# Optimization experiments

Hardware: AMD Instinct MI355X
Metric: run time of the kernel (lower is better)

The kernel has to match this reference:

```python
import jax, jax.numpy as jnp
import numpy as np

INPUT_SIZE = 1024
HIDDEN_SIZE = 1024
BATCH = 4096


def setup_inputs() -> dict:
    key = jax.random.key(0)
    ks = jax.random.split(key, 20)
    k = 1.0 / HIDDEN_SIZE
    bound = float(np.sqrt(k))

    def u(kk, shape):
        return jax.random.uniform(kk, shape, jnp.float32, -bound, bound)

    inp = {
        "x": jax.random.normal(ks[0], (BATCH, INPUT_SIZE), jnp.float32),
        "h0": jax.random.normal(ks[1], (BATCH, HIDDEN_SIZE), jnp.float32),
        "c0": jax.random.normal(ks[2], (BATCH, HIDDEN_SIZE), jnp.float32),
        "W_ii": u(ks[3], (INPUT_SIZE, HIDDEN_SIZE)), "b_ii": u(ks[4], (HIDDEN_SIZE,)),
        "W_if": u(ks[5], (INPUT_SIZE, HIDDEN_SIZE)), "b_if": u(ks[6], (HIDDEN_SIZE,)),
        "W_ig": u(ks[7], (INPUT_SIZE, HIDDEN_SIZE)), "b_ig": u(ks[8], (HIDDEN_SIZE,)),
        "W_io": u(ks[9], (INPUT_SIZE, HIDDEN_SIZE)), "b_io": u(ks[10], (HIDDEN_SIZE,)),
        "W_hi": u(ks[11], (HIDDEN_SIZE, HIDDEN_SIZE)), "b_hi": u(ks[12], (HIDDEN_SIZE,)),
        "W_hf": u(ks[13], (HIDDEN_SIZE, HIDDEN_SIZE)), "b_hf": u(ks[14], (HIDDEN_SIZE,)),
        "W_hg": u(ks[15], (HIDDEN_SIZE, HIDDEN_SIZE)), "b_hg": u(ks[16], (HIDDEN_SIZE,)),
        "W_ho": u(ks[17], (HIDDEN_SIZE, HIDDEN_SIZE)), "b_ho": u(ks[18], (HIDDEN_SIZE,)),
    }
    return inp


def reference(x, h0, c0,
              W_ii, b_ii, W_if, b_if, W_ig, b_ig, W_io, b_io,
              W_hi, b_hi, W_hf, b_hf, W_hg, b_hg, W_ho, b_ho):
    # Fuse the 4 input-side and 4 hidden-side GEMMs into two wide GEMMs,
    # then a single fused gate computation — same math as the original.
    Wi = jnp.concatenate([W_ii, W_if, W_ig, W_io], axis=1)  # [In, 4H]
    Wh = jnp.concatenate([W_hi, W_hf, W_hg, W_ho], axis=1)  # [H, 4H]
    b = jnp.concatenate([b_ii + b_hi, b_if + b_hf, b_ig + b_hg, b_io + b_ho])
    gates = x @ Wi + h0 @ Wh + b  # [B, 4H]
    zi, zf, zg, zo = jnp.split(gates, 4, axis=1)
    i = jax.nn.sigmoid(zi)
    f = jax.nn.sigmoid(zf)
    g = jnp.tanh(zg)
    o = jax.nn.sigmoid(zo)
    c1 = f * c0 + i * g
    h1 = o * c1
    return h1, c1
```

## Files before the change

kernel.cpp:

```cpp
#include <hip/hip_runtime.h>

typedef unsigned short u16;
typedef unsigned int u32;
typedef __attribute__((ext_vector_type(8))) short short8;
typedef __attribute__((ext_vector_type(4))) float f32x4;

__device__ __forceinline__ u16 f2b(float f) {
  u32 u = __builtin_bit_cast(u32, f);
  u32 r = (u + 0x7FFFu + ((u >> 16) & 1u)) >> 16;
  return (u16)r;
}

__device__ __forceinline__ void gl_lds16(const void* g, void* l) {
  __builtin_amdgcn_global_load_lds(
      (const __attribute__((address_space(1))) u32*)g,
      (__attribute__((address_space(3))) u32*)l, 16, 0, 0);
}

struct Ptrs8 { const float* p[8]; };

__global__ __launch_bounds__(256) void wt_pack(Ptrs8 w, u16* __restrict__ Wt) {
  __shared__ float lds[64 * 64];
  const int tid = threadIdx.x;
  const int bid = blockIdx.x;
  const int mat = bid >> 8;
  const int g = mat & 3, h = mat >> 2;
  const int tile = bid & 255;
  const int kt = tile >> 4, nt = tile & 15;
  const float* __restrict__ src = w.p[mat];

#pragma unroll
  for (int i = 0; i < 4; ++i) {
    int c = tid + i * 256;
    int k = c >> 4, n4 = (c & 15) * 4;
    gl_lds16(src + (size_t)(kt * 64 + k) * 1024 + nt * 64 + n4, &lds[c * 4]);
  }
  asm volatile("s_waitcnt vmcnt(0)");
  __syncthreads();

#pragma unroll
  for (int i = 0; i < 2; ++i) {
    int c = tid + i * 256;
    int n = c & 63, kb = (c >> 6) * 8;
    short8 v;
#pragma unroll
    for (int j = 0; j < 8; ++j) v[j] = (short)f2b(lds[(kb + j) * 64 + n]);
    size_t off = (size_t)(g * 1024 + nt * 64 + n) * 2048 + h * 1024 + kt * 64 + kb;
    *reinterpret_cast<short8*>(Wt + off) = v;
  }
}

__global__ __launch_bounds__(256) void xh_pack(const float* __restrict__ x,
                                               const float* __restrict__ h0,
                                               u16* __restrict__ Ap) {
  int t = blockIdx.x * 256 + threadIdx.x;
  int m = t >> 8, kc = t & 255;
  const float* src = (kc < 128) ? (x + (size_t)m * 1024 + kc * 8)
                                : (h0 + (size_t)m * 1024 + (kc - 128) * 8);
  float4 a = *reinterpret_cast<const float4*>(src);
  float4 b = *reinterpret_cast<const float4*>(src + 4);
  short8 v;
  v[0] = (short)f2b(a.x); v[1] = (short)f2b(a.y);
  v[2] = (short)f2b(a.z); v[3] = (short)f2b(a.w);
  v[4] = (short)f2b(b.x); v[5] = (short)f2b(b.y);
  v[6] = (short)f2b(b.z); v[7] = (short)f2b(b.w);
  *reinterpret_cast<short8*>(Ap + (size_t)m * 2048 + kc * 8) = v;
}

__global__ void bias_pack(Ptrs8 b, float* __restrict__ bias) {
  int i = blockIdx.x * 1024 + threadIdx.x;
  int g = i >> 10, n = i & 1023;
  bias[i] = b.p[g][n] + b.p[4 + g][n];
}

#define LD8(base, off) (*reinterpret_cast<const short8*>((base) + (off)))
#define MFMA_(a, b, c) __builtin_amdgcn_mfma_f32_16x16x32_bf16(a, b, c, 0, 0, 0)

#define READ_A(DST, BASE)                                   \
  _Pragma("unroll")                                         \
  for (int mi = 0; mi < 4; ++mi) {                          \
    DST[mi][0] = LD8(Ab, arow + (BASE + mi) * 1024 + c0k);  \
    DST[mi][1] = LD8(Ab, arow + (BASE + mi) * 1024 + c1k);  \
  }
#define READ_B(DST, GB)                                     \
  _Pragma("unroll")                                         \
  for (int g = 0; g < 2; ++g) {                             \
    DST[g][0] = LD8(Bb, bbase + (GB + g) * 4096 + c0k);     \
    DST[g][1] = LD8(Bb, bbase + (GB + g) * 4096 + c1k);     \
  }
#define MFMA_QUAD(AF, BF, MO, GO)                                              \
  _Pragma("unroll")                                                            \
  for (int mi = 0; mi < 4; ++mi)                                               \
    _Pragma("unroll")                                                          \
    for (int g = 0; g < 2; ++g) {                                              \
      acc[MO + mi][GO + g] = MFMA_(AF[mi][0], BF[g][0], acc[MO + mi][GO + g]); \
      acc[MO + mi][GO + g] = MFMA_(AF[mi][1], BF[g][1], acc[MO + mi][GO + g]); \
    }

__global__ __launch_bounds__(512, 2) void lstm_fused(
    const u16* __restrict__ Ap, const float* __restrict__ c0,
    const u16* __restrict__ Wt, const float* __restrict__ bias,
    float* __restrict__ out) {
  __shared__ u16 As[2][256 * 64];
  __shared__ u16 Bs[2][256 * 64];

  const int tid = threadIdx.x;
  const int lane = tid & 63;
  const int wid = tid >> 6;
  const int wr = wid >> 2;
  const int wc = wid & 3;
  const int fl = lane & 15;
  const int hi = lane >> 4;
  const int lo7 = fl & 7;

  const int bid0 = blockIdx.x;
  const int sbid = (bid0 & 7) * 32 + (bid0 >> 3);
  const int m0 = (sbid >> 4) * 256;
  const int n0 = (sbid & 15) * 64;

  int aoff[4], boff[4];
#pragma unroll
  for (int i = 0; i < 4; ++i) {
    const int L = tid + i * 512;
    const int r = L >> 3, cL = L & 7;
    const int cg = cL ^ (r & 7);
    aoff[i] = (m0 + r) * 2048 + cg * 8;
    const int ge = r >> 6, wce = (r >> 4) & 3, ue = r & 15;
    boff[i] = (ge * 1024 + n0 + wce * 16 + ue) * 2048 + cg * 8;
  }

  auto stage = [&](int buf, int t) {
    const int k0 = t * 64;
#pragma unroll
    for (int i = 0; i < 4; ++i)
      gl_lds16(Ap + aoff[i] + k0, &As[buf][(tid + i * 512) * 8]);
#pragma unroll
    for (int i = 0; i < 4; ++i)
      gl_lds16(Wt + boff[i] + k0, &Bs[buf][(tid + i * 512) * 8]);
  };

  const int c0k = (hi ^ lo7) * 8;
  const int c1k = ((4 + hi) ^ lo7) * 8;
  const int arow = (wr * 128 + fl) * 64;
  const int bbase = (wc * 16 + fl) * 64;

  f32x4 acc[8][4] = {};

  stage(0, 0);

  for (int t = 0; t < 32; ++t) {
    const int cur = t & 1, nxt = cur ^ 1;
    const u16* Ab = &As[cur][0];
    const u16* Bb = &Bs[cur][0];

    asm volatile("s_waitcnt vmcnt(0)" ::: "memory");
    __builtin_amdgcn_s_barrier();

    short8 af03[4][2], af47[4][2], bf01[2][2], bf23[2][2];
    READ_B(bf01, 0)
    READ_A(af03, 0)
    READ_A(af47, 4)
    READ_B(bf23, 2)

    if (t < 31) stage(nxt, t + 1);

    MFMA_QUAD(af03, bf01, 0, 0)
    MFMA_QUAD(af47, bf01, 4, 0)
    MFMA_QUAD(af03, bf23, 0, 2)
    MFMA_QUAD(af47, bf23, 4, 2)
  }

  const int col = n0 + wc * 16 + fl;
  float bv[4];
#pragma unroll
  for (int g = 0; g < 4; ++g) bv[g] = bias[g * 1024 + col];

#pragma unroll
  for (int mi = 0; mi < 8; ++mi) {
#pragma unroll
    for (int r = 0; r < 4; ++r) {
      const int row = m0 + wr * 128 + mi * 16 + hi * 4 + r;
      const float zi = acc[mi][0][r] + bv[0];
      const float zf = acc[mi][1][r] + bv[1];
      const float zg = acc[mi][2][r] + bv[2];
      const float zo = acc[mi][3][r] + bv[3];
      const float ig = 1.f / (1.f + __expf(-zi));
      const float fg = 1.f / (1.f + __expf(-zf));
      const float gg = 1.f - 2.f / (__expf(2.f * zg) + 1.f);
      const float og = 1.f / (1.f + __expf(-zo));
      const float c0v = c0[(size_t)row * 1024 + col];
      const float c1 = fg * c0v + ig * gg;
      const float h1 = og * c1;
      out[(size_t)row * 1024 + col] = h1;
      out[(size_t)4194304 + (size_t)row * 1024 + col] = c1;
    }
  }
}

extern "C" void kernel_launch(void* const* d_in, const int* in_sizes, int n_in,
                              void* d_out, int out_size, void* d_ws, size_t ws_size,
                              hipStream_t stream) {
  const float* x  = (const float*)d_in[0];
  const float* h0 = (const float*)d_in[1];
  const float* c0 = (const float*)d_in[2];
  Ptrs8 w, b;
  for (int i = 0; i < 4; ++i) {
    w.p[i]     = (const float*)d_in[3 + 2 * i];
    b.p[i]     = (const float*)d_in[4 + 2 * i];
    w.p[4 + i] = (const float*)d_in[11 + 2 * i];
    b.p[4 + i] = (const float*)d_in[12 + 2 * i];
  }
  u16* Wt = (u16*)d_ws;
  u16* Ap = (u16*)((char*)d_ws + (size_t)4096 * 2048 * 2);
  float* bias = (float*)((char*)d_ws + (size_t)2 * 4096 * 2048 * 2);
  float* out = (float*)d_out;

  wt_pack<<<2048, 256, 0, stream>>>(w, Wt);
  xh_pack<<<4096, 256, 0, stream>>>(x, h0, Ap);
  bias_pack<<<4, 1024, 0, stream>>>(b, bias);
  lstm_fused<<<256, 512, 0, stream>>>(Ap, c0, Wt, bias, out);
}
```

Measured before the change: 94.39 us.

## Restructure GEMM main loop into phased ping-pong with split staging and priority

Replaces the simple double-buffered K loop, which waited on all loads, with a two-tile-ahead prefetch in the same buffer. Each K-tile is split into four MFMA phases separated by barriers. Global-to-LDS loads are split into halves and interleaved between the phases, partial vmcnt waits keep loads in flight, and s_setprio raises wave priority during MFMA bursts. The aim is to overlap memory latency with matrix math and keep waves in lockstep, at the cost of many extra barriers.

```diff
diff --git a/kernel.cpp b/kernel.cpp
--- a/kernel.cpp
+++ b/kernel.cpp
@@ -75,6 +75,11 @@
 
 #define LD8(base, off) (*reinterpret_cast<const short8*>((base) + (off)))
 #define MFMA_(a, b, c) __builtin_amdgcn_mfma_f32_16x16x32_bf16(a, b, c, 0, 0, 0)
+#define PIN asm volatile("" ::: "memory")
+#define SB0 __builtin_amdgcn_sched_barrier(0)
+#define BARR __builtin_amdgcn_s_barrier()
+#define PRIO1 __builtin_amdgcn_s_setprio(1);
+#define PRIO0 __builtin_amdgcn_s_setprio(0);
 
 #define READ_A(DST, BASE)                                   \
   _Pragma("unroll")                                         \
@@ -97,6 +102,42 @@
       acc[MO + mi][GO + g] = MFMA_(AF[mi][1], BF[g][1], acc[MO + mi][GO + g]); \
     }
 
+#define TILE4(BUF, T, ST, TAILW)                                             \
+  {                                                                          \
+    const u16* Ab = &As[BUF][0];                                             \
+    const u16* Bb = &Bs[BUF][0];                                             \
+    short8 af03[4][2], af47[4][2], bf01[2][2], bf23[2][2];                   \
+                                               \
+    READ_A(af03, 0) READ_B(bf01, 0) PIN;                                     \
+    BARR;                                                                    \
+    asm volatile("s_waitcnt lgkmcnt(0)"); SB0;                               \
+    PRIO1 MFMA_QUAD(af03, bf01, 0, 0) PRIO0                                  \
+    BARR; PIN;                                                               \
+                                 \
+    READ_B(bf23, 2) PIN;                                                     \
+    if (ST) { stageA(BUF, (T) + 2, 0); stageB(BUF, (T) + 2, 0); }            \
+    PIN;                                                                     \
+    BARR;                                                                    \
+    asm volatile("s_waitcnt lgkmcnt(0)"); SB0;                               \
+    PRIO1 MFMA_QUAD(af03, bf23, 0, 2) PRIO0                                  \
+    BARR; PIN;                                                               \
+                                     \
+    READ_A(af47, 4) PIN;                                                     \
+    if (ST) { stageB(BUF, (T) + 2, 1); }                                     \
+    PIN;                                                                     \
+    BARR;                                                                    \
+    asm volatile("s_waitcnt lgkmcnt(0)"); SB0;                               \
+    PRIO1 MFMA_QUAD(af47, bf01, 4, 0) PRIO0                                  \
+    BARR; PIN;                                                               \
+                                       \
+    if (ST) { stageA(BUF, (T) + 2, 1); }                                     \
+    PIN;                                                                     \
+    PRIO1 MFMA_QUAD(af47, bf23, 4, 2) PRIO0                                  \
+    if ((TAILW) == 8) asm volatile("s_waitcnt vmcnt(8)" ::: "memory");       \
+    else if ((TAILW) == 0) asm volatile("s_waitcnt vmcnt(0)" ::: "memory");  \
+    BARR; PIN;                                                               \
+  }
+
 __global__ __launch_bounds__(512, 2) void lstm_fused(
     const u16* __restrict__ Ap, const float* __restrict__ c0,
     const u16* __restrict__ Wt, const float* __restrict__ bias,
@@ -129,14 +170,15 @@
     boff[i] = (ge * 1024 + n0 + wce * 16 + ue) * 2048 + cg * 8;
   }
 
-  auto stage = [&](int buf, int t) {
+  auto stageA = [&](int buf, int t, int h) {
     const int k0 = t * 64;
-#pragma unroll
-    for (int i = 0; i < 4; ++i)
-      gl_lds16(Ap + aoff[i] + k0, &As[buf][(tid + i * 512) * 8]);
-#pragma unroll
-    for (int i = 0; i < 4; ++i)
-      gl_lds16(Wt + boff[i] + k0, &Bs[buf][(tid + i * 512) * 8]);
+    gl_lds16(Ap + aoff[h] + k0, &As[buf][(tid + h * 512) * 8]);
+    gl_lds16(Ap + aoff[h + 2] + k0, &As[buf][(tid + (h + 2) * 512) * 8]);
+  };
+  auto stageB = [&](int buf, int t, int h) {
+    const int k0 = t * 64;
+    gl_lds16(Wt + boff[2 * h] + k0, &Bs[buf][(tid + (2 * h) * 512) * 8]);
+    gl_lds16(Wt + boff[2 * h + 1] + k0, &Bs[buf][(tid + (2 * h + 1) * 512) * 8]);
   };
 
   const int c0k = (hi ^ lo7) * 8;
@@ -146,29 +188,17 @@
 
   f32x4 acc[8][4] = {};
 
-  stage(0, 0);
-
-  for (int t = 0; t < 32; ++t) {
-    const int cur = t & 1, nxt = cur ^ 1;
-    const u16* Ab = &As[cur][0];
-    const u16* Bb = &Bs[cur][0];
-
-    asm volatile("s_waitcnt vmcnt(0)" ::: "memory");
-    __builtin_amdgcn_s_barrier();
-
-    short8 af03[4][2], af47[4][2], bf01[2][2], bf23[2][2];
-    READ_B(bf01, 0)
-    READ_A(af03, 0)
-    READ_A(af47, 4)
-    READ_B(bf23, 2)
-
-    if (t < 31) stage(nxt, t + 1);
-
-    MFMA_QUAD(af03, bf01, 0, 0)
-    MFMA_QUAD(af47, bf01, 4, 0)
-    MFMA_QUAD(af03, bf23, 0, 2)
-    MFMA_QUAD(af47, bf23, 4, 2)
-  }
+  stageA(0, 0, 0); stageB(0, 0, 0); stageB(0, 0, 1); stageA(0, 0, 1);
+  stageA(1, 1, 0); stageB(1, 1, 0); stageB(1, 1, 1); stageA(1, 1, 1);
+  asm volatile("s_waitcnt vmcnt(8)" ::: "memory");
+  BARR; PIN;
+
+  for (int i = 0; i < 15; ++i) {
+    TILE4(0, 2 * i, 1, 8)
+    TILE4(1, 2 * i + 1, 1, 8)
+  }
+  TILE4(0, 30, 0, 0)
+  TILE4(1, 31, 0, -1)
 
   const int col = n0 + wc * 16 + fl;
   float bv[4];
```

Result: no change. 92.72 us (-1.8%).

## Merge pack kernels and retile LSTM GEMM with triple-buffered K=32 pipeline

Applied to the files above, without the earlier changes.

Folds the three prepack kernels into one launch so there is less launch overhead. Retiles the fused GEMM to 256-thread blocks of 256x32 outputs (512 blocks) with K-steps of 32, and replaces double buffering with a three-stage LDS ring that keeps two loads in flight under a partial vmcnt wait. The aim is more blocks for occupancy and better latency hiding. In exchange there are twice as many barriers, each K-step does less MFMA work, and the narrower N tile lowers B reuse per block.

```diff
diff --git a/kernel.cpp b/kernel.cpp
--- a/kernel.cpp
+++ b/kernel.cpp
@@ -19,155 +19,149 @@
 
 struct Ptrs8 { const float* p[8]; };
 
-__global__ __launch_bounds__(256) void wt_pack(Ptrs8 w, u16* __restrict__ Wt) {
+__global__ __launch_bounds__(256) void prepack(Ptrs8 w, Ptrs8 b,
+                                               const float* __restrict__ x,
+                                               const float* __restrict__ h0,
+                                               u16* __restrict__ Wt,
+                                               u16* __restrict__ Ap,
+                                               float* __restrict__ bias) {
   __shared__ float lds[64 * 64];
   const int tid = threadIdx.x;
   const int bid = blockIdx.x;
-  const int mat = bid >> 8;
-  const int g = mat & 3, h = mat >> 2;
-  const int tile = bid & 255;
-  const int kt = tile >> 4, nt = tile & 15;
-  const float* __restrict__ src = w.p[mat];
-
-#pragma unroll
-  for (int i = 0; i < 4; ++i) {
-    int c = tid + i * 256;
-    int k = c >> 4, n4 = (c & 15) * 4;
-    gl_lds16(src + (size_t)(kt * 64 + k) * 1024 + nt * 64 + n4, &lds[c * 4]);
-  }
-  asm volatile("s_waitcnt vmcnt(0)");
-  __syncthreads();
-
-#pragma unroll
-  for (int i = 0; i < 2; ++i) {
-    int c = tid + i * 256;
-    int n = c & 63, kb = (c >> 6) * 8;
+
+  if (bid < 2048) {
+    const int mat = bid >> 8;
+    const int g = mat & 3, h = mat >> 2;
+    const int tile = bid & 255;
+    const int kt = tile >> 4, nt = tile & 15;
+    const float* __restrict__ src = w.p[mat];
+#pragma unroll
+    for (int i = 0; i < 4; ++i) {
+      int c = tid + i * 256;
+      int k = c >> 4, n4 = (c & 15) * 4;
+      gl_lds16(src + (size_t)(kt * 64 + k) * 1024 + nt * 64 + n4, &lds[c * 4]);
+    }
+    asm volatile("s_waitcnt vmcnt(0)");
+    __syncthreads();
+#pragma unroll
+    for (int i = 0; i < 2; ++i) {
+      int c = tid + i * 256;
+      int n = c & 63, kb = (c >> 6) * 8;
+      short8 v;
+#pragma unroll
+      for (int j = 0; j < 8; ++j) v[j] = (short)f2b(lds[(kb + j) * 64 + n]);
+      size_t off = (size_t)(g * 1024 + nt * 64 + n) * 2048 + h * 1024 + kt * 64 + kb;
+      *reinterpret_cast<short8*>(Wt + off) = v;
+    }
+  } else if (bid < 6144) {
+    int t = (bid - 2048) * 256 + tid;
+    int m = t >> 8, kc = t & 255;
+    const float* src = (kc < 128) ? (x + (size_t)m * 1024 + kc * 8)
+                                  : (h0 + (size_t)m * 1024 + (kc - 128) * 8);
+    float4 a = *reinterpret_cast<const float4*>(src);
+    float4 bb = *reinterpret_cast<const float4*>(src + 4);
     short8 v;
-#pragma unroll
-    for (int j = 0; j < 8; ++j) v[j] = (short)f2b(lds[(kb + j) * 64 + n]);
-    size_t off = (size_t)(g * 1024 + nt * 64 + n) * 2048 + h * 1024 + kt * 64 + kb;
-    *reinterpret_cast<short8*>(Wt + off) = v;
-  }
-}
-
-__global__ __launch_bounds__(256) void xh_pack(const float* __restrict__ x,
-                                               const float* __restrict__ h0,
-                                               u16* __restrict__ Ap) {
-  int t = blockIdx.x * 256 + threadIdx.x;
-  int m = t >> 8, kc = t & 255;
-  const float* src = (kc < 128) ? (x + (size_t)m * 1024 + kc * 8)
-                                : (h0 + (size_t)m * 1024 + (kc - 128) * 8);
-  float4 a = *reinterpret_cast<const float4*>(src);
-  float4 b = *reinterpret_cast<const float4*>(src + 4);
-  short8 v;
-  v[0] = (short)f2b(a.x); v[1] = (short)f2b(a.y);
-  v[2] = (short)f2b(a.z); v[3] = (short)f2b(a.w);
-  v[4] = (short)f2b(b.x); v[5] = (short)f2b(b.y);
-  v[6] = (short)f2b(b.z); v[7] = (short)f2b(b.w);
-  *reinterpret_cast<short8*>(Ap + (size_t)m * 2048 + kc * 8) = v;
-}
-
-__global__ void bias_pack(Ptrs8 b, float* __restrict__ bias) {
-  int i = blockIdx.x * 1024 + threadIdx.x;
-  int g = i >> 10, n = i & 1023;
-  bias[i] = b.p[g][n] + b.p[4 + g][n];
+    v[0] = (short)f2b(a.x); v[1] = (short)f2b(a.y);
+    v[2] = (short)f2b(a.z); v[3] = (short)f2b(a.w);
+    v[4] = (short)f2b(bb.x); v[5] = (short)f2b(bb.y);
+    v[6] = (short)f2b(bb.z); v[7] = (short)f2b(bb.w);
+    *reinterpret_cast<short8*>(Ap + (size_t)m * 2048 + kc * 8) = v;
+  } else {
+    int i = (bid - 6144) * 256 + tid;
+    int g = i >> 10, n = i & 1023;
+    bias[i] = b.p[g][n] + b.p[4 + g][n];
+  }
 }
 
 #define LD8(base, off) (*reinterpret_cast<const short8*>((base) + (off)))
 #define MFMA_(a, b, c) __builtin_amdgcn_mfma_f32_16x16x32_bf16(a, b, c, 0, 0, 0)
 
-#define READ_A(DST, BASE)                                   \
-  _Pragma("unroll")                                         \
-  for (int mi = 0; mi < 4; ++mi) {                          \
-    DST[mi][0] = LD8(Ab, arow + (BASE + mi) * 1024 + c0k);  \
-    DST[mi][1] = LD8(Ab, arow + (BASE + mi) * 1024 + c1k);  \
-  }
-#define READ_B(DST, GB)                                     \
-  _Pragma("unroll")                                         \
-  for (int g = 0; g < 2; ++g) {                             \
-    DST[g][0] = LD8(Bb, bbase + (GB + g) * 4096 + c0k);     \
-    DST[g][1] = LD8(Bb, bbase + (GB + g) * 4096 + c1k);     \
-  }
-#define MFMA_QUAD(AF, BF, MO, GO)                                              \
-  _Pragma("unroll")                                                            \
-  for (int mi = 0; mi < 4; ++mi)                                               \
-    _Pragma("unroll")                                                          \
-    for (int g = 0; g < 2; ++g) {                                              \
-      acc[MO + mi][GO + g] = MFMA_(AF[mi][0], BF[g][0], acc[MO + mi][GO + g]); \
-      acc[MO + mi][GO + g] = MFMA_(AF[mi][1], BF[g][1], acc[MO + mi][GO + g]); \
-    }
-
-__global__ __launch_bounds__(512, 2) void lstm_fused(
+__global__ __launch_bounds__(256, 2) void lstm_fused(
     const u16* __restrict__ Ap, const float* __restrict__ c0,
     const u16* __restrict__ Wt, const float* __restrict__ bias,
     float* __restrict__ out) {
-  __shared__ u16 As[2][256 * 64];
-  __shared__ u16 Bs[2][256 * 64];
+  __shared__ u16 As[3][256 * 32];
+  __shared__ u16 Bs[3][128 * 32];
 
   const int tid = threadIdx.x;
   const int lane = tid & 63;
   const int wid = tid >> 6;
-  const int wr = wid >> 2;
-  const int wc = wid & 3;
+  const int wr = wid >> 1;
+  const int wc = wid & 1;
   const int fl = lane & 15;
   const int hi = lane >> 4;
-  const int lo7 = fl & 7;
 
   const int bid0 = blockIdx.x;
-  const int sbid = (bid0 & 7) * 32 + (bid0 >> 3);
-  const int m0 = (sbid >> 4) * 256;
-  const int n0 = (sbid & 15) * 64;
-
-  int aoff[4], boff[4];
+  const int sbid = (bid0 & 7) * 64 + (bid0 >> 3);
+  const int m0 = (sbid >> 5) * 256;
+  const int n0 = (sbid & 31) * 32;
+
+  int aoff[4], boff[2];
 #pragma unroll
   for (int i = 0; i < 4; ++i) {
-    const int L = tid + i * 512;
-    const int r = L >> 3, cL = L & 7;
-    const int cg = cL ^ (r & 7);
-    aoff[i] = (m0 + r) * 2048 + cg * 8;
-    const int ge = r >> 6, wce = (r >> 4) & 3, ue = r & 15;
+    const int c = tid + i * 256;
+    const int row = c >> 2, cL = c & 3;
+    const int cg = cL ^ ((row >> 2) & 3);
+    aoff[i] = (m0 + row) * 2048 + cg * 8;
+  }
+#pragma unroll
+  for (int i = 0; i < 2; ++i) {
+    const int c = tid + i * 256;
+    const int row = c >> 2, cL = c & 3;
+    const int cg = cL ^ ((row >> 2) & 3);
+    const int ge = row >> 5, rem = row & 31;
+    const int wce = rem >> 4, ue = rem & 15;
     boff[i] = (ge * 1024 + n0 + wce * 16 + ue) * 2048 + cg * 8;
   }
 
   auto stage = [&](int buf, int t) {
-    const int k0 = t * 64;
+    const int k0 = t * 32;
 #pragma unroll
     for (int i = 0; i < 4; ++i)
-      gl_lds16(Ap + aoff[i] + k0, &As[buf][(tid + i * 512) * 8]);
-#pragma unroll
-    for (int i = 0; i < 4; ++i)
-      gl_lds16(Wt + boff[i] + k0, &Bs[buf][(tid + i * 512) * 8]);
+      gl_lds16(Ap + aoff[i] + k0, &As[buf][(tid + i * 256) * 8]);
+#pragma unroll
+    for (int i = 0; i < 2; ++i)
+      gl_lds16(Wt + boff[i] + k0, &Bs[buf][(tid + i * 256) * 8]);
   };
 
-  const int c0k = (hi ^ lo7) * 8;
-  const int c1k = ((4 + hi) ^ lo7) * 8;
-  const int arow = (wr * 128 + fl) * 64;
-  const int bbase = (wc * 16 + fl) * 64;
+  const int cks = (hi ^ ((fl >> 2) & 3)) * 8;
+  const int arow = (wr * 128 + fl) * 32;
+  const int brow = (wc * 16 + fl) * 32;
 
   f32x4 acc[8][4] = {};
 
   stage(0, 0);
-
-  for (int t = 0; t < 32; ++t) {
-    const int cur = t & 1, nxt = cur ^ 1;
+  stage(1, 1);
+
+  int cur = 0;
+  for (int t = 0; t < 64; ++t) {
+    if (t < 62) {
+      asm volatile("s_waitcnt vmcnt(6)" ::: "memory");
+    } else {
+      asm volatile("s_waitcnt vmcnt(0)" ::: "memory");
+    }
+    __builtin_amdgcn_s_barrier();
+
     const u16* Ab = &As[cur][0];
     const u16* Bb = &Bs[cur][0];
-
-    asm volatile("s_waitcnt vmcnt(0)" ::: "memory");
-    __builtin_amdgcn_s_barrier();
-
-    short8 af03[4][2], af47[4][2], bf01[2][2], bf23[2][2];
-    READ_B(bf01, 0)
-    READ_A(af03, 0)
-    READ_A(af47, 4)
-    READ_B(bf23, 2)
-
-    if (t < 31) stage(nxt, t + 1);
-
-    MFMA_QUAD(af03, bf01, 0, 0)
-    MFMA_QUAD(af47, bf01, 4, 0)
-    MFMA_QUAD(af03, bf23, 0, 2)
-    MFMA_QUAD(af47, bf23, 4, 2)
+    short8 af[8], bf[4];
+#pragma unroll
+    for (int mi = 0; mi < 8; ++mi) af[mi] = LD8(Ab, arow + mi * 512 + cks);
+#pragma unroll
+    for (int g = 0; g < 4; ++g) bf[g] = LD8(Bb, brow + g * 1024 + cks);
+
+    if (t < 62) {
+      const int sb = (cur >= 1) ? cur - 1 : cur + 2;
+      stage(sb, t + 2);
+    }
+
+#pragma unroll
+    for (int mi = 0; mi < 8; ++mi)
+#pragma unroll
+      for (int g = 0; g < 4; ++g)
+        acc[mi][g] = MFMA_(af[mi], bf[g], acc[mi][g]);
+
+    cur = (cur >= 2) ? 0 : cur + 1;
   }
 
   const int col = n0 + wc * 16 + fl;
@@ -215,8 +209,6 @@
   float* bias = (float*)((char*)d_ws + (size_t)2 * 4096 * 2048 * 2);
   float* out = (float*)d_out;
 
-  wt_pack<<<2048, 256, 0, stream>>>(w, Wt);
-  xh_pack<<<4096, 256, 0, stream>>>(x, h0, Ap);
-  bias_pack<<<4, 1024, 0, stream>>>(b, bias);
-  lstm_fused<<<256, 512, 0, stream>>>(Ap, c0, Wt, bias, out);
-}
+  prepack<<<6160, 256, 0, stream>>>(w, b, x, h0, Wt, Ap, bias);
+  lstm_fused<<<512, 256, 0, stream>>>(Ap, c0, Wt, bias, out);
+}
```

Result: slower. 97.60 us (+3.4%).

## Load B fragments straight from global into registers and merge pack kernels

Applied to the files above, without the earlier changes.

The GEMM kernel stops staging the weight tile in LDS. Each wave now loads its B fragments directly from global memory into registers with inline asm, double-buffered across k-steps, while A stays staged through LDS. The block-to-tile mapping is swapped so neighbouring blocks share weight columns, and the three pre-pack kernels are merged into one launch to cut launch overhead. The changes halve LDS use and remove B LDS traffic, at the cost of more VGPRs and redundant global B loads across waves that share columns.

```diff
diff --git a/kernel.cpp b/kernel.cpp
--- a/kernel.cpp
+++ b/kernel.cpp
@@ -19,62 +19,64 @@
 
 struct Ptrs8 { const float* p[8]; };
 
-__global__ __launch_bounds__(256) void wt_pack(Ptrs8 w, u16* __restrict__ Wt) {
+__global__ __launch_bounds__(256) void prepack(Ptrs8 w, Ptrs8 b,
+                                               const float* __restrict__ x,
+                                               const float* __restrict__ h0,
+                                               u16* __restrict__ Wt,
+                                               u16* __restrict__ Ap,
+                                               float* __restrict__ bias) {
   __shared__ float lds[64 * 64];
   const int tid = threadIdx.x;
   const int bid = blockIdx.x;
-  const int mat = bid >> 8;
-  const int g = mat & 3, h = mat >> 2;
-  const int tile = bid & 255;
-  const int kt = tile >> 4, nt = tile & 15;
-  const float* __restrict__ src = w.p[mat];
-
-#pragma unroll
-  for (int i = 0; i < 4; ++i) {
-    int c = tid + i * 256;
-    int k = c >> 4, n4 = (c & 15) * 4;
-    gl_lds16(src + (size_t)(kt * 64 + k) * 1024 + nt * 64 + n4, &lds[c * 4]);
-  }
-  asm volatile("s_waitcnt vmcnt(0)");
-  __syncthreads();
-
-#pragma unroll
-  for (int i = 0; i < 2; ++i) {
-    int c = tid + i * 256;
-    int n = c & 63, kb = (c >> 6) * 8;
+
+  if (bid < 2048) {
+    const int mat = bid >> 8;
+    const int g = mat & 3, h = mat >> 2;
+    const int tile = bid & 255;
+    const int kt = tile >> 4, nt = tile & 15;
+    const float* __restrict__ src = w.p[mat];
+#pragma unroll
+    for (int i = 0; i < 4; ++i) {
+      int c = tid + i * 256;
+      int k = c >> 4, n4 = (c & 15) * 4;
+      gl_lds16(src + (size_t)(kt * 64 + k) * 1024 + nt * 64 + n4, &lds[c * 4]);
+    }
+    asm volatile("s_waitcnt vmcnt(0)");
+    __syncthreads();
+#pragma unroll
+    for (int i = 0; i < 2; ++i) {
+      int c = tid + i * 256;
+      int n = c & 63, kb = (c >> 6) * 8;
+      short8 v;
+#pragma unroll
+      for (int j = 0; j < 8; ++j) v[j] = (short)f2b(lds[(kb + j) * 64 + n]);
+      size_t off = (size_t)(g * 1024 + nt * 64 + n) * 2048 + h * 1024 + kt * 64 + kb;
+      *reinterpret_cast<short8*>(Wt + off) = v;
+    }
+  } else if (bid < 6144) {
+    int t = (bid - 2048) * 256 + tid;
+    int m = t >> 8, kc = t & 255;
+    const float* src = (kc < 128) ? (x + (size_t)m * 1024 + kc * 8)
+                                  : (h0 + (size_t)m * 1024 + (kc - 128) * 8);
+    float4 a = *reinterpret_cast<const float4*>(src);
+    float4 bb = *reinterpret_cast<const float4*>(src + 4);
     short8 v;
-#pragma unroll
-    for (int j = 0; j < 8; ++j) v[j] = (short)f2b(lds[(kb + j) * 64 + n]);
-    size_t off = (size_t)(g * 1024 + nt * 64 + n) * 2048 + h * 1024 + kt * 64 + kb;
-    *reinterpret_cast<short8*>(Wt + off) = v;
-  }
-}
-
-__global__ __launch_bounds__(256) void xh_pack(const float* __restrict__ x,
-                                               const float* __restrict__ h0,
-                                               u16* __restrict__ Ap) {
-  int t = blockIdx.x * 256 + threadIdx.x;
-  int m = t >> 8, kc = t & 255;
-  const float* src = (kc < 128) ? (x + (size_t)m * 1024 + kc * 8)
-                                : (h0 + (size_t)m * 1024 + (kc - 128) * 8);
-  float4 a = *reinterpret_cast<const float4*>(src);
-  float4 b = *reinterpret_cast<const float4*>(src + 4);
-  short8 v;
-  v[0] = (short)f2b(a.x); v[1] = (short)f2b(a.y);
-  v[2] = (short)f2b(a.z); v[3] = (short)f2b(a.w);
-  v[4] = (short)f2b(b.x); v[5] = (short)f2b(b.y);
-  v[6] = (short)f2b(b.z); v[7] = (short)f2b(b.w);
-  *reinterpret_cast<short8*>(Ap + (size_t)m * 2048 + kc * 8) = v;
-}
-
-__global__ void bias_pack(Ptrs8 b, float* __restrict__ bias) {
-  int i = blockIdx.x * 1024 + threadIdx.x;
-  int g = i >> 10, n = i & 1023;
-  bias[i] = b.p[g][n] + b.p[4 + g][n];
+    v[0] = (short)f2b(a.x); v[1] = (short)f2b(a.y);
+    v[2] = (short)f2b(a.z); v[3] = (short)f2b(a.w);
+    v[4] = (short)f2b(bb.x); v[5] = (short)f2b(bb.y);
+    v[6] = (short)f2b(bb.z); v[7] = (short)f2b(bb.w);
+    *reinterpret_cast<short8*>(Ap + (size_t)m * 2048 + kc * 8) = v;
+  } else {
+    int i = (bid - 6144) * 256 + tid;
+    int g = i >> 10, n = i & 1023;
+    bias[i] = b.p[g][n] + b.p[4 + g][n];
+  }
 }
 
 #define LD8(base, off) (*reinterpret_cast<const short8*>((base) + (off)))
 #define MFMA_(a, b, c) __builtin_amdgcn_mfma_f32_16x16x32_bf16(a, b, c, 0, 0, 0)
+#define BARR __builtin_amdgcn_s_barrier()
+#define SB0 __builtin_amdgcn_sched_barrier(0)
 
 #define READ_A(DST, BASE)                                   \
   _Pragma("unroll")                                         \
@@ -82,27 +84,46 @@
     DST[mi][0] = LD8(Ab, arow + (BASE + mi) * 1024 + c0k);  \
     DST[mi][1] = LD8(Ab, arow + (BASE + mi) * 1024 + c1k);  \
   }
-#define READ_B(DST, GB)                                     \
-  _Pragma("unroll")                                         \
-  for (int g = 0; g < 2; ++g) {                             \
-    DST[g][0] = LD8(Bb, bbase + (GB + g) * 4096 + c0k);     \
-    DST[g][1] = LD8(Bb, bbase + (GB + g) * 4096 + c1k);     \
-  }
-#define MFMA_QUAD(AF, BF, MO, GO)                                              \
-  _Pragma("unroll")                                                            \
-  for (int mi = 0; mi < 4; ++mi)                                               \
-    _Pragma("unroll")                                                          \
-    for (int g = 0; g < 2; ++g) {                                              \
-      acc[MO + mi][GO + g] = MFMA_(AF[mi][0], BF[g][0], acc[MO + mi][GO + g]); \
-      acc[MO + mi][GO + g] = MFMA_(AF[mi][1], BF[g][1], acc[MO + mi][GO + g]); \
-    }
+
+#define MFMA_HALF(AF, BF, MO)                                                \
+  _Pragma("unroll")                                                          \
+  for (int mi = 0; mi < 4; ++mi)                                             \
+    _Pragma("unroll")                                                        \
+    for (int g = 0; g < 4; ++g) {                                            \
+      acc[MO + mi][g] = MFMA_(AF[mi][0], BF[g][0], acc[MO + mi][g]);         \
+      acc[MO + mi][g] = MFMA_(AF[mi][1], BF[g][1], acc[MO + mi][g]);         \
+    }
+
+#define LOADB(BF, T)                                                         \
+  _Pragma("unroll")                                                          \
+  for (int g = 0; g < 4; ++g) {                                              \
+    const u16* p = gb[g] + (size_t)(T) * 64;                                 \
+    asm volatile("global_load_dwordx4 %0, %2, off\n\t"                       \
+                 "global_load_dwordx4 %1, %2, off offset:64"                 \
+                 : "=v"(BF[g][0]), "=v"(BF[g][1])                            \
+                 : "v"(p));                                                  \
+  }
+
+#define TILEX(CUR, T, BFC, BFN, DOLOAD, DOSTAGE, WCNT)                       \
+  {                                                                          \
+    const u16* Ab = &As[CUR][0];                                             \
+    if (DOLOAD) { LOADB(BFN, (T) + 1) }                                      \
+    asm volatile("s_waitcnt vmcnt(" #WCNT ")" ::: "memory");                 \
+    BARR;                                                                    \
+    SB0;                                                                     \
+    if (DOSTAGE) stageA((CUR) ^ 1, (T) + 1);                                 \
+    short8 af[4][2];                                                         \
+    READ_A(af, 0)                                                            \
+    MFMA_HALF(af, BFC, 0)                                                    \
+    READ_A(af, 4)                                                            \
+    MFMA_HALF(af, BFC, 4)                                                    \
+  }
 
 __global__ __launch_bounds__(512, 2) void lstm_fused(
     const u16* __restrict__ Ap, const float* __restrict__ c0,
     const u16* __restrict__ Wt, const float* __restrict__ bias,
     float* __restrict__ out) {
   __shared__ u16 As[2][256 * 64];
-  __shared__ u16 Bs[2][256 * 64];
 
   const int tid = threadIdx.x;
   const int lane = tid & 63;
@@ -115,60 +136,45 @@
 
   const int bid0 = blockIdx.x;
   const int sbid = (bid0 & 7) * 32 + (bid0 >> 3);
-  const int m0 = (sbid >> 4) * 256;
-  const int n0 = (sbid & 15) * 64;
-
-  int aoff[4], boff[4];
+  const int m0 = (sbid & 15) * 256;
+  const int n0 = (sbid >> 4) * 64;
+
+  int aoff[4];
 #pragma unroll
   for (int i = 0; i < 4; ++i) {
     const int L = tid + i * 512;
     const int r = L >> 3, cL = L & 7;
     const int cg = cL ^ (r & 7);
     aoff[i] = (m0 + r) * 2048 + cg * 8;
-    const int ge = r >> 6, wce = (r >> 4) & 3, ue = r & 15;
-    boff[i] = (ge * 1024 + n0 + wce * 16 + ue) * 2048 + cg * 8;
-  }
-
-  auto stage = [&](int buf, int t) {
+  }
+  auto stageA = [&](int buf, int t) {
     const int k0 = t * 64;
 #pragma unroll
     for (int i = 0; i < 4; ++i)
       gl_lds16(Ap + aoff[i] + k0, &As[buf][(tid + i * 512) * 8]);
-#pragma unroll
-    for (int i = 0; i < 4; ++i)
-      gl_lds16(Wt + boff[i] + k0, &Bs[buf][(tid + i * 512) * 8]);
   };
+
+  const u16* gb[4];
+#pragma unroll
+  for (int g = 0; g < 4; ++g)
+    gb[g] = Wt + (size_t)(g * 1024 + n0 + wc * 16 + fl) * 2048 + hi * 8;
 
   const int c0k = (hi ^ lo7) * 8;
   const int c1k = ((4 + hi) ^ lo7) * 8;
   const int arow = (wr * 128 + fl) * 64;
-  const int bbase = (wc * 16 + fl) * 64;
 
   f32x4 acc[8][4] = {};
-
-  stage(0, 0);
-
-  for (int t = 0; t < 32; ++t) {
-    const int cur = t & 1, nxt = cur ^ 1;
-    const u16* Ab = &As[cur][0];
-    const u16* Bb = &Bs[cur][0];
-
-    asm volatile("s_waitcnt vmcnt(0)" ::: "memory");
-    __builtin_amdgcn_s_barrier();
-
-    short8 af03[4][2], af47[4][2], bf01[2][2], bf23[2][2];
-    READ_B(bf01, 0)
-    READ_A(af03, 0)
-    READ_A(af47, 4)
-    READ_B(bf23, 2)
-
-    if (t < 31) stage(nxt, t + 1);
-
-    MFMA_QUAD(af03, bf01, 0, 0)
-    MFMA_QUAD(af47, bf01, 4, 0)
-    MFMA_QUAD(af03, bf23, 0, 2)
-    MFMA_QUAD(af47, bf23, 4, 2)
-  }
+  short8 bfA[4][2], bfB[4][2];
+
+  stageA(0, 0);
+  LOADB(bfA, 0)
+
+  for (int i = 0; i < 15; ++i) {
+    TILEX(0, 2 * i, bfA, bfB, 1, 1, 8)
+    TILEX(1, 2 * i + 1, bfB, bfA, 1, 1, 8)
+  }
+  TILEX(0, 30, bfA, bfB, 1, 1, 8)
+  TILEX(1, 31, bfB, bfA, 0, 0, 0)
 
   const int col = n0 + wc * 16 + fl;
   float bv[4];
@@ -215,8 +221,6 @@
   float* bias = (float*)((char*)d_ws + (size_t)2 * 4096 * 2048 * 2);
   float* out = (float*)d_out;
 
-  wt_pack<<<2048, 256, 0, stream>>>(w, Wt);
-  xh_pack<<<4096, 256, 0, stream>>>(x, h0, Ap);
-  bias_pack<<<4, 1024, 0, stream>>>(b, bias);
+  prepack<<<6160, 256, 0, stream>>>(w, b, x, h0, Wt, Ap, bias);
   lstm_fused<<<256, 512, 0, stream>>>(Ap, c0, Wt, bias, out);
 }
```

Result: slower. 105.6 us (+11.9%).
